# Performance work log

Hardware: AMD Instinct MI355X
Metric: run time of the kernel (lower is better)

## Reference

```python
import jax, jax.numpy as jnp
import numpy as np

N1 = 100000  # source cloud size (x1)
N2 = 100000  # target cloud size (x2)
F = 64       # point feature dim
E = 1600000  # number of radius edges (avg 16 neighbors)
H = 128      # MLP hidden/out dim


def setup_inputs() -> dict:
    key = jax.random.key(0)
    ks = jax.random.split(key, 12)
    s = 0.05
    return {
        "x1_features": jax.random.normal(ks[0], (N1, F), jnp.float32),
        "x1_pos": jax.random.normal(ks[1], (N1, 3), jnp.float32),
        "x2_features": jax.random.normal(ks[2], (N2, F), jnp.float32),
        "x2_pos": jax.random.normal(ks[3], (N2, 3), jnp.float32),
        "W1": jax.random.normal(ks[4], (2 * F + 3, H), jnp.float32) * s,
        "b1": jnp.zeros((H,), jnp.float32),
        "W2": jax.random.normal(ks[5], (H, H), jnp.float32) * s,
        "b2": jnp.zeros((H,), jnp.float32),
        "W3": jax.random.normal(ks[6], (H, H), jnp.float32) * s,
        "b3": jnp.zeros((H,), jnp.float32),
        "edge_src": jax.random.randint(ks[7], (E,), 0, N1, jnp.int32),
        "edge_dst": jax.random.randint(ks[8], (E,), 0, N2, jnp.int32),
    }


def reference(x1_features, x1_pos, x2_features, x2_pos,
              W1, b1, W2, b2, W3, b3, edge_src, edge_dst):
    # message(x_i, x_j, pos_i, pos_j): i = target (x2, edge_dst), j = source (x1, edge_src)
    # msg = cat([x_i, x_j, pos_j - pos_i], dim=1)  -> [E, 2F+3]
    msg = jnp.concatenate(
        [x2_features[edge_dst],
         x1_features[edge_src],
         x1_pos[edge_src] - x2_pos[edge_dst]], axis=1)
    # MLP (Linear+ReLU x3, FastFlow3D make_mlp style)
    h = jax.nn.relu(msg @ W1 + b1)
    h = jax.nn.relu(h @ W2 + b2)
    h = jax.nn.relu(h @ W3 + b3)
    # scatter-max aggregation onto x2 nodes; PyG fills empty segments with 0
    out = jax.ops.segment_max(h, edge_dst, num_segments=N2)
    out = jnp.where(jnp.isneginf(out), 0.0, out)
    return out, x2_pos
```

## Files before the change

kernel.cpp:

```cpp
#include <hip/hip_runtime.h>
#include <hip/hip_bf16.h>

#define DEV __device__ __forceinline__

typedef short bf16x8 __attribute__((ext_vector_type(8)));
typedef float f32x16 __attribute__((ext_vector_type(16)));

static constexpr int FDIM  = 64;
static constexpr int HH    = 128;
static constexpr int K1RAW = 2 * FDIM + 3;
static constexpr int K1    = 144;
static constexpr int KS1   = K1 / 16;
static constexpr int KS2   = HH / 16;
static constexpr int TM    = 128;

static constexpr int CSTR  = TM * 16 + 16;
static constexpr int HCH   = 16;
static constexpr int HBUF  = HCH * CSTR;
static constexpr int L_TOT = 2 * HBUF + TM * 4;

static constexpr int WT1_ELEMS = HH * K1;
static constexpr int WT2_ELEMS = HH * HH;
static constexpr int WT_TOTAL  = WT1_ELEMS + 2 * WT2_ELEMS;

DEV unsigned pack2(float a, float b) {
    union { __hip_bfloat162 h; unsigned u; } cv;
    cv.h.x = __float2bfloat16(a);
    cv.h.y = __float2bfloat16(b);
    return cv.u;
}
DEV unsigned short f2bf(float f) {
    union { __hip_bfloat16 h; unsigned short u; } cv;
    cv.h = __float2bfloat16(f);
    return cv.u;
}

__global__ void k_cvt(const float* __restrict__ src, unsigned short* __restrict__ dst, int n8) {
    int i = blockIdx.x * 256 + threadIdx.x;
    if (i < n8) {
        float4 a = *(const float4*)(src + (size_t)i * 8);
        float4 b = *(const float4*)(src + (size_t)i * 8 + 4);
        uint4 o;
        o.x = pack2(a.x, a.y); o.y = pack2(a.z, a.w);
        o.z = pack2(b.x, b.y); o.w = pack2(b.z, b.w);
        *(uint4*)(dst + (size_t)i * 8) = o;
    }
}

__global__ void k_wprep(const float* __restrict__ W1, const float* __restrict__ W2,
                        const float* __restrict__ W3, unsigned short* __restrict__ wt) {
    int i = blockIdx.x * 256 + threadIdx.x;
    if (i < WT1_ELEMS) {
        int n = i / K1, k = i % K1;
        float v = (k < K1RAW) ? W1[k * HH + n] : 0.f;
        wt[i] = f2bf(v);
    } else if (i < WT1_ELEMS + WT2_ELEMS) {
        int j = i - WT1_ELEMS; int n = j / HH, k = j % HH;
        wt[i] = f2bf(W2[k * HH + n]);
    } else if (i < WT_TOTAL) {
        int j = i - WT1_ELEMS - WT2_ELEMS; int n = j / HH, k = j % HH;
        wt[i] = f2bf(W3[k * HH + n]);
    }
}

__global__ void k_hist(const int* __restrict__ edst, int* __restrict__ cnt, int E) {
    int e = blockIdx.x * 256 + threadIdx.x;
    if (e < E) atomicAdd(&cnt[edst[e]], 1);
}

__global__ void k_scan_part(const int* __restrict__ cnt, int* __restrict__ partial, int n2) {
    __shared__ int sm[256];
    int t = threadIdx.x;
    int base = blockIdx.x * 1024 + t * 4;
    int s = 0;
#pragma unroll
    for (int j = 0; j < 4; j++) { int idx = base + j; if (idx < n2) s += cnt[idx]; }
    sm[t] = s; __syncthreads();
    for (int off = 128; off > 0; off >>= 1) {
        if (t < off) sm[t] += sm[t + off];
        __syncthreads();
    }
    if (t == 0) partial[blockIdx.x] = sm[0];
}

__global__ void k_scan_top(int* __restrict__ partial, int nb) {
    __shared__ int sm[256];
    int t = threadIdx.x;
    int v = (t < nb) ? partial[t] : 0;
    sm[t] = v; __syncthreads();
    for (int off = 1; off < 256; off <<= 1) {
        int add = (t >= off) ? sm[t - off] : 0;
        __syncthreads();
        sm[t] += add;
        __syncthreads();
    }
    if (t < nb) partial[t] = sm[t] - v;
}

__global__ void k_scan_down(const int* __restrict__ cnt, const int* __restrict__ partial,
                            int* __restrict__ cursor, int n2) {
    __shared__ int sm[256];
    int t = threadIdx.x;
    int base = blockIdx.x * 1024 + t * 4;
    int c[4]; int s = 0;
#pragma unroll
    for (int j = 0; j < 4; j++) { int idx = base + j; c[j] = (idx < n2) ? cnt[idx] : 0; s += c[j]; }
    sm[t] = s; __syncthreads();
    for (int off = 1; off < 256; off <<= 1) {
        int add = (t >= off) ? sm[t - off] : 0;
        __syncthreads();
        sm[t] += add;
        __syncthreads();
    }
    int run = partial[blockIdx.x] + (sm[t] - s);
#pragma unroll
    for (int j = 0; j < 4; j++) {
        int idx = base + j;
        if (idx < n2) cursor[idx] = run;
        run += c[j];
    }
}

__global__ void k_fill(const int* __restrict__ edst, const int* __restrict__ esrc,
                       int* __restrict__ cursor,
                       int* __restrict__ csr_s, int* __restrict__ csr_d, int E) {
    int e = blockIdx.x * 256 + threadIdx.x;
    if (e < E) {
        int d = edst[e];
        int p = atomicAdd(&cursor[d], 1);
        csr_s[p] = esrc[e];
        csr_d[p] = d;
    }
}

DEV f32x16 zerov() {
    f32x16 v;
#pragma unroll
    for (int i = 0; i < 16; i++) v[i] = 0.f;
    return v;
}

template <int KSTEPS>
DEV void load_A(const unsigned short* __restrict__ wtl, int rt, int l31, int hh, bf16x8* A) {
#pragma unroll
    for (int ks = 0; ks < KSTEPS; ks++)
        A[ks] = *(const bf16x8*)(wtl + (rt * 32 + l31) * (KSTEPS * 16) + ks * 16 + 8 * hh);
}

template <int KSTEPS>
DEV f32x16 tile_mfma(const bf16x8* A, const char* __restrict__ srcrow) {
    f32x16 acc = zerov();
#pragma unroll
    for (int ks = 0; ks < KSTEPS; ks++) {
        bf16x8 B = *(const bf16x8*)(srcrow + 2 * ks * CSTR);
        acc = __builtin_amdgcn_mfma_f32_32x32x16_bf16(A[ks], B, acc, 0, 0, 0);
    }
    return acc;
}

DEV void tile_store(const f32x16& acc, const float* __restrict__ bias, char* __restrict__ dstrow,
                    int rt, int hh) {
#pragma unroll
    for (int g = 0; g < 4; g++) {
        float4 bv = *(const float4*)(bias + rt * 32 + 8 * g + 4 * hh);
        float v0 = fmaxf(acc[4 * g + 0] + bv.x, 0.f);
        float v1 = fmaxf(acc[4 * g + 1] + bv.y, 0.f);
        float v2 = fmaxf(acc[4 * g + 2] + bv.z, 0.f);
        float v3 = fmaxf(acc[4 * g + 3] + bv.w, 0.f);
        uint2 w; w.x = pack2(v0, v1); w.y = pack2(v2, v3);
        *(uint2*)(dstrow + g * CSTR) = w;
    }
}

template <bool SORTED, bool BF16SRC>
__global__ __launch_bounds__(512, 4) void k_main(
    const float* __restrict__ x1f, const float* __restrict__ x1p,
    const float* __restrict__ x2f, const float* __restrict__ x2p,
    const char* __restrict__ xb1, const char* __restrict__ xb2,
    const float* __restrict__ b1, const float* __restrict__ b2, const float* __restrict__ b3,
    const unsigned short* __restrict__ wt,
    const int* __restrict__ csr_s, const int* __restrict__ csr_d,
    const int* __restrict__ edge_src, const int* __restrict__ edge_dst,
    float* __restrict__ out, int E) {
    __shared__ __align__(16) char sm[L_TOT];
    char* hA = sm;
    char* hB = sm + HBUF;
    int*  dl = (int*)(sm + 2 * HBUF);

    const int tid  = threadIdx.x;
    const int lane = tid & 63;
    const int wv   = tid >> 6;
    const int l31  = lane & 31;
    const int hh   = lane >> 5;
    const int eb   = blockIdx.x * TM;

    if (tid < TM) {
        const int slot = eb + tid;
        dl[tid] = (slot < E) ? (SORTED ? csr_d[slot] : edge_dst[slot]) : -1;
    }

    const int rt  = wv & 3;
    const int ct0 = (wv >> 2) * 2;
    bf16x8 A[KS1];

    load_A<KS1>(wt, rt, l31, hh, A);
#pragma unroll
    for (int j = 0; j < 2; j++) {
        const int r = (ct0 + j) * 32 + l31;
        const int slot = eb + r;
        const bool ok = slot < E;
        int d = 0, s = 0;
        if (ok) {
            d = SORTED ? csr_d[slot] : edge_dst[slot];
            s = SORTED ? csr_s[slot] : edge_src[slot];
        }
        bf16x8 Bv[KS1];
        if (BF16SRC) {
            const char* bx2 = xb2 + (size_t)d * (2 * FDIM);
            const char* bx1 = xb1 + (size_t)s * (2 * FDIM);
#pragma unroll
            for (int ks = 0; ks < 4; ks++)
                Bv[ks] = *(const bf16x8*)(bx2 + (2 * ks + hh) * 16);
#pragma unroll
            for (int ks = 4; ks < 8; ks++)
                Bv[ks] = *(const bf16x8*)(bx1 + (2 * ks + hh) * 16 - 128);
        } else {
            const float* fx2 = x2f + (size_t)d * FDIM;
            const float* fx1 = x1f + (size_t)s * FDIM;
#pragma unroll
            for (int ks = 0; ks < 8; ks++) {
                const float* b = (ks < 4) ? (fx2 + (2 * ks + hh) * 8)
                                          : (fx1 + (2 * ks + hh) * 8 - 64);
                float4 a0 = *(const float4*)(b);
                float4 a1 = *(const float4*)(b + 4);
                union { unsigned u[4]; bf16x8 v; } B;
                B.u[0] = pack2(a0.x, a0.y); B.u[1] = pack2(a0.z, a0.w);
                B.u[2] = pack2(a1.x, a1.y); B.u[3] = pack2(a1.z, a1.w);
                Bv[ks] = B.v;
            }
        }
        {
            float dx = 0.f, dy = 0.f, dz = 0.f;
            if (ok) {
                dx = x1p[s * 3 + 0] - x2p[d * 3 + 0];
                dy = x1p[s * 3 + 1] - x2p[d * 3 + 1];
                dz = x1p[s * 3 + 2] - x2p[d * 3 + 2];
            }
            union { unsigned u[4]; bf16x8 v; } P;
            P.u[0] = hh ? 0u : pack2(dx, dy);
            P.u[1] = hh ? 0u : pack2(dz, 0.f);
            P.u[2] = 0u; P.u[3] = 0u;
            Bv[8] = P.v;
        }
        f32x16 acc = zerov();
#pragma unroll
        for (int ks = 0; ks < KS1; ks++)
            acc = __builtin_amdgcn_mfma_f32_32x32x16_bf16(A[ks], Bv[ks], acc, 0, 0, 0);
        tile_store(acc, b1, hA + r * 16 + 8 * hh + (4 * rt) * CSTR, rt, hh);
    }
    __syncthreads();

    load_A<KS2>(wt + WT1_ELEMS, rt, l31, hh, A);
#pragma unroll
    for (int j = 0; j < 2; j++) {
        const int r = (ct0 + j) * 32 + l31;
        f32x16 acc = tile_mfma<KS2>(A, hA + r * 16 + hh * CSTR);
        tile_store(acc, b2, hB + r * 16 + 8 * hh + (4 * rt) * CSTR, rt, hh);
    }
    __syncthreads();

    load_A<KS2>(wt + WT1_ELEMS + WT2_ELEMS, rt, l31, hh, A);
#pragma unroll
    for (int j = 0; j < 2; j++) {
        const int r = (ct0 + j) * 32 + l31;
        f32x16 acc = tile_mfma<KS2>(A, hB + r * 16 + hh * CSTR);
        tile_store(acc, b3, hA + r * 16 + 8 * hh + (4 * rt) * CSTR, rt, hh);
    }
    __syncthreads();

    {
        const int p     = tid & 63;
        const int strip = tid >> 6;
        const int r0 = strip * 16;
        const char* fbase = hA + (p >> 2) * CSTR + (p & 3) * 4;
        int curd = dl[r0];
        int rs = r0;
        float m0 = 0.f, m1 = 0.f;
#pragma unroll
        for (int r = r0; r < r0 + 16; r++) {
            int d = dl[r];
            if (d != curd) {
                if (curd >= 0) {
                    bool extL = (rs == r0) && (r0 == 0 || dl[r0 - 1] == curd);
                    if (extL) {
                        if (m0 > 0.f) atomicMax((int*)out + (size_t)curd * HH + 2 * p,     __float_as_int(m0));
                        if (m1 > 0.f) atomicMax((int*)out + (size_t)curd * HH + 2 * p + 1, __float_as_int(m1));
                    } else {
                        out[(size_t)curd * HH + 2 * p]     = m0;
                        out[(size_t)curd * HH + 2 * p + 1] = m1;
                    }
                }
                curd = d; rs = r; m0 = 0.f; m1 = 0.f;
            }
            unsigned w = *(const unsigned*)(fbase + r * 16);
            m0 = fmaxf(m0, __uint_as_float(w << 16));
            m1 = fmaxf(m1, __uint_as_float(w & 0xffff0000u));
        }
        if (curd >= 0) {
            bool extL = (rs == r0) && (r0 == 0 || dl[r0 - 1] == curd);
            bool extR = (r0 + 16 == TM) || (dl[r0 + 16] == curd);
            if (extL || extR) {
                if (m0 > 0.f) atomicMax((int*)out + (size_t)curd * HH + 2 * p,     __float_as_int(m0));
                if (m1 > 0.f) atomicMax((int*)out + (size_t)curd * HH + 2 * p + 1, __float_as_int(m1));
            } else {
                out[(size_t)curd * HH + 2 * p]     = m0;
                out[(size_t)curd * HH + 2 * p + 1] = m1;
            }
        }
    }
}

extern "C" void kernel_launch(void* const* d_in, const int* in_sizes, int n_in,
                              void* d_out, int out_size, void* d_ws, size_t ws_size,
                              hipStream_t stream) {
    const float* x1f = (const float*)d_in[0];
    const float* x1p = (const float*)d_in[1];
    const float* x2f = (const float*)d_in[2];
    const float* x2p = (const float*)d_in[3];
    const float* W1  = (const float*)d_in[4];
    const float* b1  = (const float*)d_in[5];
    const float* W2  = (const float*)d_in[6];
    const float* b2  = (const float*)d_in[7];
    const float* W3  = (const float*)d_in[8];
    const float* b3  = (const float*)d_in[9];
    const int* esrc  = (const int*)d_in[10];
    const int* edst  = (const int*)d_in[11];
    const int E  = in_sizes[10];
    const int N1 = in_sizes[1] / 3;
    const int N2 = in_sizes[3] / 3;
    float* out = (float*)d_out;

    size_t off = 0;
    auto take = [&](size_t bytes) { size_t o = off; off = (off + bytes + 255) & ~(size_t)255; return o; };
    size_t o_cnt = take(4 * (size_t)N2);
    size_t o_cur = take(4 * (size_t)N2);
    size_t o_par = take(4 * 256);
    size_t o_cs  = take(4 * (size_t)E);
    size_t o_cd  = take(4 * (size_t)E);
    size_t o_wt  = take(2 * (size_t)WT_TOTAL);
    size_t need_csr = off;
    size_t o_x1  = take(2 * (size_t)N1 * FDIM);
    size_t o_x2  = take(2 * (size_t)N2 * FDIM);
    size_t need_bf = off;

    const int NB = (N2 + 1023) / 1024;
    bool use_csr = (need_csr <= ws_size) && (NB <= 256);
    bool use_bf  = (need_bf <= ws_size);

    char* ws = (char*)d_ws;
    unsigned short* wt = use_csr ? (unsigned short*)(ws + o_wt) : (unsigned short*)ws;
    int* cnt    = (int*)(ws + o_cnt);
    int* cursor = (int*)(ws + o_cur);
    int* part   = (int*)(ws + o_par);
    int* csr_s  = (int*)(ws + o_cs);
    int* csr_d  = (int*)(ws + o_cd);
    char* xb1   = ws + o_x1;
    char* xb2   = ws + o_x2;

    (void)hipMemsetAsync(out, 0, (size_t)N2 * HH * 4, stream);
    (void)hipMemcpyAsync(out + (size_t)N2 * HH, x2p, (size_t)N2 * 3 * 4,
                         hipMemcpyDeviceToDevice, stream);

    k_wprep<<<(WT_TOTAL + 255) / 256, 256, 0, stream>>>(W1, W2, W3, wt);

    if (use_bf) {
        int n8_1 = N1 * FDIM / 8, n8_2 = N2 * FDIM / 8;
        k_cvt<<<(n8_1 + 255) / 256, 256, 0, stream>>>(x1f, (unsigned short*)xb1, n8_1);
        k_cvt<<<(n8_2 + 255) / 256, 256, 0, stream>>>(x2f, (unsigned short*)xb2, n8_2);
    }

    const int grid = (E + TM - 1) / TM;
    if (use_csr) {
        (void)hipMemsetAsync(cnt, 0, 4 * (size_t)N2, stream);
        k_hist<<<(E + 255) / 256, 256, 0, stream>>>(edst, cnt, E);
        k_scan_part<<<NB, 256, 0, stream>>>(cnt, part, N2);
        k_scan_top<<<1, 256, 0, stream>>>(part, NB);
        k_scan_down<<<NB, 256, 0, stream>>>(cnt, part, cursor, N2);
        k_fill<<<(E + 255) / 256, 256, 0, stream>>>(edst, esrc, cursor, csr_s, csr_d, E);
        if (use_bf)
            k_main<true, true><<<grid, 512, 0, stream>>>(
                x1f, x1p, x2f, x2p, xb1, xb2, b1, b2, b3, wt, csr_s, csr_d, esrc, edst, out, E);
        else
            k_main<true, false><<<grid, 512, 0, stream>>>(
                x1f, x1p, x2f, x2p, xb1, xb2, b1, b2, b3, wt, csr_s, csr_d, esrc, edst, out, E);
    } else {
        if (use_bf)
            k_main<false, true><<<grid, 512, 0, stream>>>(
                x1f, x1p, x2f, x2p, xb1, xb2, b1, b2, b3, wt, edst, edst, esrc, edst, out, E);
        else
            k_main<false, false><<<grid, 512, 0, stream>>>(
                x1f, x1p, x2f, x2p, xb1, xb2, b1, b2, b3, wt, edst, edst, esrc, edst, out, E);
    }
}
```

Before: 664.5 us.

## Make main kernel persistent with register-prefetched gathers of the next tile

The main MLP kernel becomes persistent, with a grid capped at 512 blocks looping over edge tiles. Each thread gathers the feature rows for the next tile into registers while the current tile's three MFMA layers run. It then stages the message matrix in shared memory coalesced, with 4 threads per row, instead of gathering straight into MFMA operand registers. The aim is to hide the gather latency behind compute. The cost is extra shared memory (a separate message buffer), more registers, an extra barrier per tile, and fewer resident blocks, which could lower occupancy.

```diff
diff --git a/kernel.cpp b/kernel.cpp
--- a/kernel.cpp
+++ b/kernel.cpp
@@ -15,13 +15,17 @@
 static constexpr int TM    = 128;
 
 static constexpr int CSTR  = TM * 16 + 16;
+static constexpr int MCH   = 18;
+static constexpr int MBUF  = MCH * CSTR;
 static constexpr int HCH   = 16;
 static constexpr int HBUF  = HCH * CSTR;
-static constexpr int L_TOT = 2 * HBUF + TM * 4;
+static constexpr int L_TOT = MBUF + HBUF + TM * 4;
 
 static constexpr int WT1_ELEMS = HH * K1;
 static constexpr int WT2_ELEMS = HH * HH;
 static constexpr int WT_TOTAL  = WT1_ELEMS + 2 * WT2_ELEMS;
+
+static constexpr int NBLK  = 512;
 
 DEV unsigned pack2(float a, float b) {
     union { __hip_bfloat162 h; unsigned u; } cv;
@@ -182,141 +186,172 @@
     const int* __restrict__ csr_s, const int* __restrict__ csr_d,
     const int* __restrict__ edge_src, const int* __restrict__ edge_dst,
     float* __restrict__ out, int E) {
-    __shared__ __align__(16) char sm[L_TOT];
-    char* hA = sm;
-    char* hB = sm + HBUF;
-    int*  dl = (int*)(sm + 2 * HBUF);
+    __shared__ __align__(16) char smem[L_TOT];
+    char* msg = smem;
+    char* hbf = smem + MBUF;
+    int*  dl  = (int*)(smem + MBUF + HBUF);
 
     const int tid  = threadIdx.x;
     const int lane = tid & 63;
     const int wv   = tid >> 6;
     const int l31  = lane & 31;
     const int hh   = lane >> 5;
-    const int eb   = blockIdx.x * TM;
-
-    if (tid < TM) {
-        const int slot = eb + tid;
-        dl[tid] = (slot < E) ? (SORTED ? csr_d[slot] : edge_dst[slot]) : -1;
-    }
-
-    const int rt  = wv & 3;
-    const int ct0 = (wv >> 2) * 2;
-    bf16x8 A[KS1];
-
-    load_A<KS1>(wt, rt, l31, hh, A);
-#pragma unroll
-    for (int j = 0; j < 2; j++) {
-        const int r = (ct0 + j) * 32 + l31;
-        const int slot = eb + r;
-        const bool ok = slot < E;
-        int d = 0, s = 0;
-        if (ok) {
-            d = SORTED ? csr_d[slot] : edge_dst[slot];
-            s = SORTED ? csr_s[slot] : edge_src[slot];
-        }
-        bf16x8 Bv[KS1];
-        if (BF16SRC) {
-            const char* bx2 = xb2 + (size_t)d * (2 * FDIM);
-            const char* bx1 = xb1 + (size_t)s * (2 * FDIM);
-#pragma unroll
-            for (int ks = 0; ks < 4; ks++)
-                Bv[ks] = *(const bf16x8*)(bx2 + (2 * ks + hh) * 16);
-#pragma unroll
-            for (int ks = 4; ks < 8; ks++)
-                Bv[ks] = *(const bf16x8*)(bx1 + (2 * ks + hh) * 16 - 128);
-        } else {
-            const float* fx2 = x2f + (size_t)d * FDIM;
-            const float* fx1 = x1f + (size_t)s * FDIM;
-#pragma unroll
-            for (int ks = 0; ks < 8; ks++) {
-                const float* b = (ks < 4) ? (fx2 + (2 * ks + hh) * 8)
-                                          : (fx1 + (2 * ks + hh) * 8 - 64);
-                float4 a0 = *(const float4*)(b);
-                float4 a1 = *(const float4*)(b + 4);
-                union { unsigned u[4]; bf16x8 v; } B;
-                B.u[0] = pack2(a0.x, a0.y); B.u[1] = pack2(a0.z, a0.w);
-                B.u[2] = pack2(a1.x, a1.y); B.u[3] = pack2(a1.z, a1.w);
-                Bv[ks] = B.v;
-            }
-        }
+    const int r    = tid >> 2;
+    const int sub  = tid & 3;
+    const int rt   = wv & 3;
+    const int ct0  = (wv >> 2) * 2;
+    const int ntiles = (E + TM - 1) / TM;
+    const int nb     = (int)gridDim.x;
+
+    auto load_idx = [&](int tile, int& d, int& s) {
+        const int slot = tile * TM + r;
+        const bool ok = (tile < ntiles) && (slot < E);
+        d = ok ? (SORTED ? csr_d[slot] : edge_dst[slot]) : -1;
+        s = ok ? (SORTED ? csr_s[slot] : edge_src[slot]) : 0;
+    };
+    auto load_feats = [&](int d, int s, uint4* v, float* pp) {
+#pragma unroll
+        for (int i = 0; i < 4; i++) { v[i].x = v[i].y = v[i].z = v[i].w = 0u; }
+        pp[0] = pp[1] = pp[2] = pp[3] = pp[4] = pp[5] = 0.f;
+        if (d >= 0) {
+            if (BF16SRC) {
+                const char* base = (sub < 2) ? (xb2 + (size_t)d * (2 * FDIM))
+                                             : (xb1 + (size_t)s * (2 * FDIM));
+#pragma unroll
+                for (int i = 0; i < 4; i++)
+                    v[i] = *(const uint4*)(base + ((sub & 1) * 4 + i) * 16);
+            } else {
+                const float* base = (sub < 2) ? (x2f + (size_t)d * FDIM)
+                                              : (x1f + (size_t)s * FDIM);
+#pragma unroll
+                for (int i = 0; i < 4; i++) {
+                    const int cc = (sub & 1) * 4 + i;
+                    float4 a = *(const float4*)(base + cc * 8);
+                    float4 b = *(const float4*)(base + cc * 8 + 4);
+                    v[i].x = pack2(a.x, a.y); v[i].y = pack2(a.z, a.w);
+                    v[i].z = pack2(b.x, b.y); v[i].w = pack2(b.z, b.w);
+                }
+            }
+            if (sub == 3) {
+                pp[0] = x1p[s * 3 + 0]; pp[1] = x1p[s * 3 + 1]; pp[2] = x1p[s * 3 + 2];
+                pp[3] = x2p[d * 3 + 0]; pp[4] = x2p[d * 3 + 1]; pp[5] = x2p[d * 3 + 2];
+            }
+        }
+    };
+
+    int tile = (int)blockIdx.x;
+    int d0, s0, d1, s1;
+    uint4 v0[4]; float p0[6];
+    load_idx(tile, d0, s0);
+    load_feats(d0, s0, v0, p0);
+    load_idx(tile + nb, d1, s1);
+
+    for (int t = tile; t < ntiles; t += nb) {
+        __syncthreads();
         {
-            float dx = 0.f, dy = 0.f, dz = 0.f;
-            if (ok) {
-                dx = x1p[s * 3 + 0] - x2p[d * 3 + 0];
-                dy = x1p[s * 3 + 1] - x2p[d * 3 + 1];
-                dz = x1p[s * 3 + 2] - x2p[d * 3 + 2];
-            }
-            union { unsigned u[4]; bf16x8 v; } P;
-            P.u[0] = hh ? 0u : pack2(dx, dy);
-            P.u[1] = hh ? 0u : pack2(dz, 0.f);
-            P.u[2] = 0u; P.u[3] = 0u;
-            Bv[8] = P.v;
-        }
-        f32x16 acc = zerov();
-#pragma unroll
-        for (int ks = 0; ks < KS1; ks++)
-            acc = __builtin_amdgcn_mfma_f32_32x32x16_bf16(A[ks], Bv[ks], acc, 0, 0, 0);
-        tile_store(acc, b1, hA + r * 16 + 8 * hh + (4 * rt) * CSTR, rt, hh);
-    }
-    __syncthreads();
-
-    load_A<KS2>(wt + WT1_ELEMS, rt, l31, hh, A);
-#pragma unroll
-    for (int j = 0; j < 2; j++) {
-        const int r = (ct0 + j) * 32 + l31;
-        f32x16 acc = tile_mfma<KS2>(A, hA + r * 16 + hh * CSTR);
-        tile_store(acc, b2, hB + r * 16 + 8 * hh + (4 * rt) * CSTR, rt, hh);
-    }
-    __syncthreads();
-
-    load_A<KS2>(wt + WT1_ELEMS + WT2_ELEMS, rt, l31, hh, A);
-#pragma unroll
-    for (int j = 0; j < 2; j++) {
-        const int r = (ct0 + j) * 32 + l31;
-        f32x16 acc = tile_mfma<KS2>(A, hB + r * 16 + hh * CSTR);
-        tile_store(acc, b3, hA + r * 16 + 8 * hh + (4 * rt) * CSTR, rt, hh);
-    }
-    __syncthreads();
-
-    {
-        const int p     = tid & 63;
-        const int strip = tid >> 6;
-        const int r0 = strip * 16;
-        const char* fbase = hA + (p >> 2) * CSTR + (p & 3) * 4;
-        int curd = dl[r0];
-        int rs = r0;
-        float m0 = 0.f, m1 = 0.f;
-#pragma unroll
-        for (int r = r0; r < r0 + 16; r++) {
-            int d = dl[r];
-            if (d != curd) {
-                if (curd >= 0) {
-                    bool extL = (rs == r0) && (r0 == 0 || dl[r0 - 1] == curd);
-                    if (extL) {
-                        if (m0 > 0.f) atomicMax((int*)out + (size_t)curd * HH + 2 * p,     __float_as_int(m0));
-                        if (m1 > 0.f) atomicMax((int*)out + (size_t)curd * HH + 2 * p + 1, __float_as_int(m1));
-                    } else {
-                        out[(size_t)curd * HH + 2 * p]     = m0;
-                        out[(size_t)curd * HH + 2 * p + 1] = m1;
+            char* colbase = msg + r * 16 + (sub * 4) * CSTR;
+#pragma unroll
+            for (int i = 0; i < 4; i++)
+                *(uint4*)(colbase + i * CSTR) = v0[i];
+            if (sub == 3) {
+                uint4 v; v.x = pack2(p0[0] - p0[3], p0[1] - p0[4]);
+                v.y = pack2(p0[2] - p0[5], 0.f); v.z = 0u; v.w = 0u;
+                *(uint4*)(msg + r * 16 + 16 * CSTR) = v;
+                uint4 z; z.x = z.y = z.z = z.w = 0u;
+                *(uint4*)(msg + r * 16 + 17 * CSTR) = z;
+            }
+            if (sub == 0) dl[r] = d0;
+        }
+        __syncthreads();
+
+        uint4 v1[4]; float p1[6];
+        load_feats(d1, s1, v1, p1);
+        int d2, s2;
+        load_idx(t + 2 * nb, d2, s2);
+
+        {
+            bf16x8 A[KS1];
+            load_A<KS1>(wt, rt, l31, hh, A);
+#pragma unroll
+            for (int j = 0; j < 2; j++) {
+                const int rr = (ct0 + j) * 32 + l31;
+                f32x16 acc = tile_mfma<KS1>(A, msg + rr * 16 + hh * CSTR);
+                tile_store(acc, b1, hbf + rr * 16 + 8 * hh + (4 * rt) * CSTR, rt, hh);
+            }
+        }
+        __syncthreads();
+
+        {
+            bf16x8 A[KS2];
+            load_A<KS2>(wt + WT1_ELEMS, rt, l31, hh, A);
+#pragma unroll
+            for (int j = 0; j < 2; j++) {
+                const int rr = (ct0 + j) * 32 + l31;
+                f32x16 acc = tile_mfma<KS2>(A, hbf + rr * 16 + hh * CSTR);
+                tile_store(acc, b2, msg + rr * 16 + 8 * hh + (4 * rt) * CSTR, rt, hh);
+            }
+        }
+        __syncthreads();
+
+        {
+            bf16x8 A[KS2];
+            load_A<KS2>(wt + WT1_ELEMS + WT2_ELEMS, rt, l31, hh, A);
+#pragma unroll
+            for (int j = 0; j < 2; j++) {
+                const int rr = (ct0 + j) * 32 + l31;
+                f32x16 acc = tile_mfma<KS2>(A, msg + rr * 16 + hh * CSTR);
+                tile_store(acc, b3, hbf + rr * 16 + 8 * hh + (4 * rt) * CSTR, rt, hh);
+            }
+        }
+        __syncthreads();
+
+        {
+            const int p     = tid & 63;
+            const int strip = tid >> 6;
+            const int r0 = strip * 16;
+            const char* fbase = hbf + (p >> 2) * CSTR + (p & 3) * 4;
+            int curd = dl[r0];
+            int rs = r0;
+            float m0 = 0.f, m1 = 0.f;
+#pragma unroll
+            for (int rr = r0; rr < r0 + 16; rr++) {
+                int d = dl[rr];
+                if (d != curd) {
+                    if (curd >= 0) {
+                        bool extL = (rs == r0) && (r0 == 0 || dl[r0 - 1] == curd);
+                        if (extL) {
+                            if (m0 > 0.f) atomicMax((int*)out + (size_t)curd * HH + 2 * p,     __float_as_int(m0));
+                            if (m1 > 0.f) atomicMax((int*)out + (size_t)curd * HH + 2 * p + 1, __float_as_int(m1));
+                        } else {
+                            out[(size_t)curd * HH + 2 * p]     = m0;
+                            out[(size_t)curd * HH + 2 * p + 1] = m1;
+                        }
                     }
+                    curd = d; rs = rr; m0 = 0.f; m1 = 0.f;
                 }
-                curd = d; rs = r; m0 = 0.f; m1 = 0.f;
-            }
-            unsigned w = *(const unsigned*)(fbase + r * 16);
-            m0 = fmaxf(m0, __uint_as_float(w << 16));
-            m1 = fmaxf(m1, __uint_as_float(w & 0xffff0000u));
-        }
-        if (curd >= 0) {
-            bool extL = (rs == r0) && (r0 == 0 || dl[r0 - 1] == curd);
-            bool extR = (r0 + 16 == TM) || (dl[r0 + 16] == curd);
-            if (extL || extR) {
-                if (m0 > 0.f) atomicMax((int*)out + (size_t)curd * HH + 2 * p,     __float_as_int(m0));
-                if (m1 > 0.f) atomicMax((int*)out + (size_t)curd * HH + 2 * p + 1, __float_as_int(m1));
-            } else {
-                out[(size_t)curd * HH + 2 * p]     = m0;
-                out[(size_t)curd * HH + 2 * p + 1] = m1;
-            }
-        }
+                unsigned w = *(const unsigned*)(fbase + rr * 16);
+                m0 = fmaxf(m0, __uint_as_float(w << 16));
+                m1 = fmaxf(m1, __uint_as_float(w & 0xffff0000u));
+            }
+            if (curd >= 0) {
+                bool extL = (rs == r0) && (r0 == 0 || dl[r0 - 1] == curd);
+                bool extR = (r0 + 16 == TM) || (dl[r0 + 16] == curd);
+                if (extL || extR) {
+                    if (m0 > 0.f) atomicMax((int*)out + (size_t)curd * HH + 2 * p,     __float_as_int(m0));
+                    if (m1 > 0.f) atomicMax((int*)out + (size_t)curd * HH + 2 * p + 1, __float_as_int(m1));
+                } else {
+                    out[(size_t)curd * HH + 2 * p]     = m0;
+                    out[(size_t)curd * HH + 2 * p + 1] = m1;
+                }
+            }
+        }
+
+        d0 = d1; s0 = s1;
+#pragma unroll
+        for (int i = 0; i < 4; i++) v0[i] = v1[i];
+#pragma unroll
+        for (int i = 0; i < 6; i++) p0[i] = p1[i];
+        d1 = d2; s1 = s2;
     }
 }
 
@@ -379,7 +414,8 @@
         k_cvt<<<(n8_2 + 255) / 256, 256, 0, stream>>>(x2f, (unsigned short*)xb2, n8_2);
     }
 
-    const int grid = (E + TM - 1) / TM;
+    const int ntiles = (E + TM - 1) / TM;
+    const int grid = (ntiles < NBLK) ? ntiles : NBLK;
     if (use_csr) {
         (void)hipMemsetAsync(cnt, 0, 4 * (size_t)N2, stream);
         k_hist<<<(E + 255) / 256, 256, 0, stream>>>(edst, cnt, E);
```

New measurement: 1.130 ms. +70.0%, slower.

## Keep MLP activations in registers and fold biases into padded weight columns

Applied to the files above, without the earlier changes.

Each wave now handles 32 edges through all three layers. Inter-layer activations stay in registers and are redistributed with cross-half-wave shuffles instead of round-tripping through LDS with block barriers. Biases are folded into an extra K column of the weight matrices, using a constant-1 input lane in the padded region. The edge tile doubles to 256 per block, with a padded LDS row layout used only for the final scatter-max. The trade-offs are heavier register pressure, weight A-fragments reloaded from global/L2 for every tile, and bias precision reduced to bf16.

```diff
diff --git a/kernel.cpp b/kernel.cpp
--- a/kernel.cpp
+++ b/kernel.cpp
@@ -8,20 +8,16 @@
 
 static constexpr int FDIM  = 64;
 static constexpr int HH    = 128;
-static constexpr int K1RAW = 2 * FDIM + 3;
-static constexpr int K1    = 144;
-static constexpr int KS1   = K1 / 16;
-static constexpr int KS2   = HH / 16;
-static constexpr int TM    = 128;
-
-static constexpr int CSTR  = TM * 16 + 16;
-static constexpr int HCH   = 16;
-static constexpr int HBUF  = HCH * CSTR;
-static constexpr int L_TOT = 2 * HBUF + TM * 4;
-
-static constexpr int WT1_ELEMS = HH * K1;
-static constexpr int WT2_ELEMS = HH * HH;
-static constexpr int WT_TOTAL  = WT1_ELEMS + 2 * WT2_ELEMS;
+static constexpr int KPAD  = 144;
+static constexpr int KS    = KPAD / 16;
+static constexpr int TM    = 256;
+
+static constexpr int CSTR  = TM * 16 + 256 + 16;
+static constexpr int HBUF  = 16 * CSTR;
+static constexpr int L_TOT = HBUF + TM * 4;
+
+static constexpr int WTL      = KPAD * HH;
+static constexpr int WT_TOTAL = 3 * WTL;
 
 DEV unsigned pack2(float a, float b) {
     union { __hip_bfloat162 h; unsigned u; } cv;
@@ -34,6 +30,7 @@
     cv.h = __float2bfloat16(f);
     return cv.u;
 }
+DEV int rowoff(int r) { return r * 16 + (r >> 3) * 8; }
 
 __global__ void k_cvt(const float* __restrict__ src, unsigned short* __restrict__ dst, int n8) {
     int i = blockIdx.x * 256 + threadIdx.x;
@@ -47,20 +44,25 @@
     }
 }
 
-__global__ void k_wprep(const float* __restrict__ W1, const float* __restrict__ W2,
-                        const float* __restrict__ W3, unsigned short* __restrict__ wt) {
+__global__ void k_wprep(const float* __restrict__ W1, const float* __restrict__ b1,
+                        const float* __restrict__ W2, const float* __restrict__ b2,
+                        const float* __restrict__ W3, const float* __restrict__ b3,
+                        unsigned short* __restrict__ wt) {
     int i = blockIdx.x * 256 + threadIdx.x;
-    if (i < WT1_ELEMS) {
-        int n = i / K1, k = i % K1;
-        float v = (k < K1RAW) ? W1[k * HH + n] : 0.f;
-        wt[i] = f2bf(v);
-    } else if (i < WT1_ELEMS + WT2_ELEMS) {
-        int j = i - WT1_ELEMS; int n = j / HH, k = j % HH;
-        wt[i] = f2bf(W2[k * HH + n]);
-    } else if (i < WT_TOTAL) {
-        int j = i - WT1_ELEMS - WT2_ELEMS; int n = j / HH, k = j % HH;
-        wt[i] = f2bf(W3[k * HH + n]);
-    }
+    if (i >= WT_TOTAL) return;
+    int layer = i / WTL, j = i % WTL;
+    int n = j / KPAD, k = j % KPAD;
+    float v = 0.f;
+    if (layer == 0) {
+        if (k < 131) v = W1[k * HH + n];
+        else if (k == 131) v = b1[n];
+    } else {
+        const float* W = (layer == 1) ? W2 : W3;
+        const float* b = (layer == 1) ? b2 : b3;
+        if (k < 128) v = W[k * HH + n];
+        else if (k == 128) v = b[n];
+    }
+    wt[i] = f2bf(v);
 }
 
 __global__ void k_hist(const int* __restrict__ edst, int* __restrict__ cnt, int E) {
@@ -139,36 +141,42 @@
     for (int i = 0; i < 16; i++) v[i] = 0.f;
     return v;
 }
-
-template <int KSTEPS>
-DEV void load_A(const unsigned short* __restrict__ wtl, int rt, int l31, int hh, bf16x8* A) {
-#pragma unroll
-    for (int ks = 0; ks < KSTEPS; ks++)
-        A[ks] = *(const bf16x8*)(wtl + (rt * 32 + l31) * (KSTEPS * 16) + ks * 16 + 8 * hh);
-}
-
-template <int KSTEPS>
-DEV f32x16 tile_mfma(const bf16x8* A, const char* __restrict__ srcrow) {
-    f32x16 acc = zerov();
-#pragma unroll
-    for (int ks = 0; ks < KSTEPS; ks++) {
-        bf16x8 B = *(const bf16x8*)(srcrow + 2 * ks * CSTR);
-        acc = __builtin_amdgcn_mfma_f32_32x32x16_bf16(A[ks], B, acc, 0, 0, 0);
-    }
-    return acc;
-}
-
-DEV void tile_store(const f32x16& acc, const float* __restrict__ bias, char* __restrict__ dstrow,
-                    int rt, int hh) {
-#pragma unroll
-    for (int g = 0; g < 4; g++) {
-        float4 bv = *(const float4*)(bias + rt * 32 + 8 * g + 4 * hh);
-        float v0 = fmaxf(acc[4 * g + 0] + bv.x, 0.f);
-        float v1 = fmaxf(acc[4 * g + 1] + bv.y, 0.f);
-        float v2 = fmaxf(acc[4 * g + 2] + bv.z, 0.f);
-        float v3 = fmaxf(acc[4 * g + 3] + bv.w, 0.f);
-        uint2 w; w.x = pack2(v0, v1); w.y = pack2(v2, v3);
-        *(uint2*)(dstrow + g * CSTR) = w;
+DEV float relu(float x) { return fmaxf(x, 0.f); }
+
+DEV void layer_reg(const unsigned short* __restrict__ wtl, const unsigned pkin[32],
+                   unsigned pkout[32], int l31, int hh, unsigned biasw) {
+    unsigned xv[16];
+#pragma unroll
+    for (int ks = 0; ks < 8; ks++) {
+        unsigned t0 = hh ? pkin[4 * ks + 0] : pkin[4 * ks + 2];
+        unsigned t1 = hh ? pkin[4 * ks + 1] : pkin[4 * ks + 3];
+        xv[2 * ks + 0] = (unsigned)__shfl_xor((int)t0, 32, 64);
+        xv[2 * ks + 1] = (unsigned)__shfl_xor((int)t1, 32, 64);
+    }
+#pragma unroll
+    for (int rt = 0; rt < 4; rt++) {
+        f32x16 acc = zerov();
+#pragma unroll
+        for (int ks = 0; ks < 8; ks++) {
+            union { unsigned u[4]; bf16x8 v; } B;
+            B.u[0] = hh ? xv[2 * ks + 0]   : pkin[4 * ks + 0];
+            B.u[1] = hh ? xv[2 * ks + 1]   : pkin[4 * ks + 1];
+            B.u[2] = hh ? pkin[4 * ks + 2] : xv[2 * ks + 0];
+            B.u[3] = hh ? pkin[4 * ks + 3] : xv[2 * ks + 1];
+            bf16x8 A = *(const bf16x8*)(wtl + (rt * 32 + l31) * KPAD + ks * 16 + 8 * hh);
+            acc = __builtin_amdgcn_mfma_f32_32x32x16_bf16(A, B.v, acc, 0, 0, 0);
+        }
+        {
+            union { unsigned u[4]; bf16x8 v; } B;
+            B.u[0] = biasw; B.u[1] = 0u; B.u[2] = 0u; B.u[3] = 0u;
+            bf16x8 A = *(const bf16x8*)(wtl + (rt * 32 + l31) * KPAD + 8 * 16 + 8 * hh);
+            acc = __builtin_amdgcn_mfma_f32_32x32x16_bf16(A, B.v, acc, 0, 0, 0);
+        }
+#pragma unroll
+        for (int g = 0; g < 4; g++) {
+            pkout[8 * rt + 2 * g + 0] = pack2(relu(acc[4 * g + 0]), relu(acc[4 * g + 1]));
+            pkout[8 * rt + 2 * g + 1] = pack2(relu(acc[4 * g + 2]), relu(acc[4 * g + 3]));
+        }
     }
 }
 
@@ -177,15 +185,13 @@
     const float* __restrict__ x1f, const float* __restrict__ x1p,
     const float* __restrict__ x2f, const float* __restrict__ x2p,
     const char* __restrict__ xb1, const char* __restrict__ xb2,
-    const float* __restrict__ b1, const float* __restrict__ b2, const float* __restrict__ b3,
     const unsigned short* __restrict__ wt,
     const int* __restrict__ csr_s, const int* __restrict__ csr_d,
     const int* __restrict__ edge_src, const int* __restrict__ edge_dst,
     float* __restrict__ out, int E) {
-    __shared__ __align__(16) char sm[L_TOT];
-    char* hA = sm;
-    char* hB = sm + HBUF;
-    int*  dl = (int*)(sm + 2 * HBUF);
+    __shared__ __align__(16) char smem[L_TOT];
+    char* hbf = smem;
+    int*  dl  = (int*)(smem + HBUF);
 
     const int tid  = threadIdx.x;
     const int lane = tid & 63;
@@ -193,103 +199,98 @@
     const int l31  = lane & 31;
     const int hh   = lane >> 5;
     const int eb   = blockIdx.x * TM;
-
-    if (tid < TM) {
-        const int slot = eb + tid;
-        dl[tid] = (slot < E) ? (SORTED ? csr_d[slot] : edge_dst[slot]) : -1;
-    }
-
-    const int rt  = wv & 3;
-    const int ct0 = (wv >> 2) * 2;
-    bf16x8 A[KS1];
-
-    load_A<KS1>(wt, rt, l31, hh, A);
-#pragma unroll
-    for (int j = 0; j < 2; j++) {
-        const int r = (ct0 + j) * 32 + l31;
-        const int slot = eb + r;
-        const bool ok = slot < E;
-        int d = 0, s = 0;
+    const int r    = wv * 32 + l31;
+    const int slot = eb + r;
+    const bool ok  = slot < E;
+
+    int d = 0, s = 0;
+    if (ok) {
+        d = SORTED ? csr_d[slot] : edge_dst[slot];
+        s = SORTED ? csr_s[slot] : edge_src[slot];
+    }
+    if (hh == 0) dl[r] = ok ? d : -1;
+
+    bf16x8 Bv[KS];
+    if (BF16SRC) {
+        const char* bx2 = xb2 + (size_t)d * (2 * FDIM);
+        const char* bx1 = xb1 + (size_t)s * (2 * FDIM);
+#pragma unroll
+        for (int ks = 0; ks < 4; ks++)
+            Bv[ks] = *(const bf16x8*)(bx2 + (2 * ks + hh) * 16);
+#pragma unroll
+        for (int ks = 4; ks < 8; ks++)
+            Bv[ks] = *(const bf16x8*)(bx1 + (2 * (ks - 4) + hh) * 16);
+    } else {
+        const float* fx2 = x2f + (size_t)d * FDIM;
+        const float* fx1 = x1f + (size_t)s * FDIM;
+#pragma unroll
+        for (int ks = 0; ks < 8; ks++) {
+            const float* b = (ks < 4) ? (fx2 + (2 * ks + hh) * 8)
+                                      : (fx1 + (2 * (ks - 4) + hh) * 8);
+            float4 a0 = *(const float4*)(b);
+            float4 a1 = *(const float4*)(b + 4);
+            union { unsigned u[4]; bf16x8 v; } B;
+            B.u[0] = pack2(a0.x, a0.y); B.u[1] = pack2(a0.z, a0.w);
+            B.u[2] = pack2(a1.x, a1.y); B.u[3] = pack2(a1.z, a1.w);
+            Bv[ks] = B.v;
+        }
+    }
+    {
+        float dx = 0.f, dy = 0.f, dz = 0.f;
         if (ok) {
-            d = SORTED ? csr_d[slot] : edge_dst[slot];
-            s = SORTED ? csr_s[slot] : edge_src[slot];
-        }
-        bf16x8 Bv[KS1];
-        if (BF16SRC) {
-            const char* bx2 = xb2 + (size_t)d * (2 * FDIM);
-            const char* bx1 = xb1 + (size_t)s * (2 * FDIM);
-#pragma unroll
-            for (int ks = 0; ks < 4; ks++)
-                Bv[ks] = *(const bf16x8*)(bx2 + (2 * ks + hh) * 16);
-#pragma unroll
-            for (int ks = 4; ks < 8; ks++)
-                Bv[ks] = *(const bf16x8*)(bx1 + (2 * ks + hh) * 16 - 128);
-        } else {
-            const float* fx2 = x2f + (size_t)d * FDIM;
-            const float* fx1 = x1f + (size_t)s * FDIM;
-#pragma unroll
-            for (int ks = 0; ks < 8; ks++) {
-                const float* b = (ks < 4) ? (fx2 + (2 * ks + hh) * 8)
-                                          : (fx1 + (2 * ks + hh) * 8 - 64);
-                float4 a0 = *(const float4*)(b);
-                float4 a1 = *(const float4*)(b + 4);
-                union { unsigned u[4]; bf16x8 v; } B;
-                B.u[0] = pack2(a0.x, a0.y); B.u[1] = pack2(a0.z, a0.w);
-                B.u[2] = pack2(a1.x, a1.y); B.u[3] = pack2(a1.z, a1.w);
-                Bv[ks] = B.v;
-            }
-        }
-        {
-            float dx = 0.f, dy = 0.f, dz = 0.f;
-            if (ok) {
-                dx = x1p[s * 3 + 0] - x2p[d * 3 + 0];
-                dy = x1p[s * 3 + 1] - x2p[d * 3 + 1];
-                dz = x1p[s * 3 + 2] - x2p[d * 3 + 2];
-            }
-            union { unsigned u[4]; bf16x8 v; } P;
-            P.u[0] = hh ? 0u : pack2(dx, dy);
-            P.u[1] = hh ? 0u : pack2(dz, 0.f);
-            P.u[2] = 0u; P.u[3] = 0u;
-            Bv[8] = P.v;
-        }
+            dx = x1p[s * 3 + 0] - x2p[d * 3 + 0];
+            dy = x1p[s * 3 + 1] - x2p[d * 3 + 1];
+            dz = x1p[s * 3 + 2] - x2p[d * 3 + 2];
+        }
+        union { unsigned u[4]; bf16x8 v; } P;
+        P.u[0] = hh ? 0u : pack2(dx, dy);
+        P.u[1] = hh ? 0u : pack2(dz, 1.0f);
+        P.u[2] = 0u; P.u[3] = 0u;
+        Bv[8] = P.v;
+    }
+
+    unsigned pkA[32], pkB[32];
+#pragma unroll
+    for (int rt = 0; rt < 4; rt++) {
         f32x16 acc = zerov();
 #pragma unroll
-        for (int ks = 0; ks < KS1; ks++)
-            acc = __builtin_amdgcn_mfma_f32_32x32x16_bf16(A[ks], Bv[ks], acc, 0, 0, 0);
-        tile_store(acc, b1, hA + r * 16 + 8 * hh + (4 * rt) * CSTR, rt, hh);
-    }
-    __syncthreads();
-
-    load_A<KS2>(wt + WT1_ELEMS, rt, l31, hh, A);
-#pragma unroll
-    for (int j = 0; j < 2; j++) {
-        const int r = (ct0 + j) * 32 + l31;
-        f32x16 acc = tile_mfma<KS2>(A, hA + r * 16 + hh * CSTR);
-        tile_store(acc, b2, hB + r * 16 + 8 * hh + (4 * rt) * CSTR, rt, hh);
-    }
-    __syncthreads();
-
-    load_A<KS2>(wt + WT1_ELEMS + WT2_ELEMS, rt, l31, hh, A);
-#pragma unroll
-    for (int j = 0; j < 2; j++) {
-        const int r = (ct0 + j) * 32 + l31;
-        f32x16 acc = tile_mfma<KS2>(A, hB + r * 16 + hh * CSTR);
-        tile_store(acc, b3, hA + r * 16 + 8 * hh + (4 * rt) * CSTR, rt, hh);
+        for (int ks = 0; ks < KS; ks++) {
+            bf16x8 A = *(const bf16x8*)(wt + (rt * 32 + l31) * KPAD + ks * 16 + 8 * hh);
+            acc = __builtin_amdgcn_mfma_f32_32x32x16_bf16(A, Bv[ks], acc, 0, 0, 0);
+        }
+#pragma unroll
+        for (int g = 0; g < 4; g++) {
+            pkA[8 * rt + 2 * g + 0] = pack2(relu(acc[4 * g + 0]), relu(acc[4 * g + 1]));
+            pkA[8 * rt + 2 * g + 1] = pack2(relu(acc[4 * g + 2]), relu(acc[4 * g + 3]));
+        }
+    }
+
+    const unsigned biasw = hh ? 0u : 0x00003F80u;
+    layer_reg(wt + WTL,     pkA, pkB, l31, hh, biasw);
+    layer_reg(wt + 2 * WTL, pkB, pkA, l31, hh, biasw);
+
+    {
+        char* dst = hbf + rowoff(r) + 8 * hh;
+#pragma unroll
+        for (int u = 0; u < 16; u++) {
+            uint2 w; w.x = pkA[2 * u + 0]; w.y = pkA[2 * u + 1];
+            *(uint2*)(dst + u * CSTR) = w;
+        }
     }
     __syncthreads();
 
     {
         const int p     = tid & 63;
         const int strip = tid >> 6;
-        const int r0 = strip * 16;
-        const char* fbase = hA + (p >> 2) * CSTR + (p & 3) * 4;
+        const int r0 = strip * 32;
+        const char* fbase = hbf + (p >> 2) * CSTR + (p & 3) * 4;
         int curd = dl[r0];
         int rs = r0;
         float m0 = 0.f, m1 = 0.f;
-#pragma unroll
-        for (int r = r0; r < r0 + 16; r++) {
-            int d = dl[r];
-            if (d != curd) {
+#pragma unroll 4
+        for (int rr = r0; rr < r0 + 32; rr++) {
+            int dd = dl[rr];
+            if (dd != curd) {
                 if (curd >= 0) {
                     bool extL = (rs == r0) && (r0 == 0 || dl[r0 - 1] == curd);
                     if (extL) {
@@ -300,15 +301,15 @@
                         out[(size_t)curd * HH + 2 * p + 1] = m1;
                     }
                 }
-                curd = d; rs = r; m0 = 0.f; m1 = 0.f;
+                curd = dd; rs = rr; m0 = 0.f; m1 = 0.f;
             }
-            unsigned w = *(const unsigned*)(fbase + r * 16);
+            unsigned w = *(const unsigned*)(fbase + rowoff(rr));
             m0 = fmaxf(m0, __uint_as_float(w << 16));
             m1 = fmaxf(m1, __uint_as_float(w & 0xffff0000u));
         }
         if (curd >= 0) {
             bool extL = (rs == r0) && (r0 == 0 || dl[r0 - 1] == curd);
-            bool extR = (r0 + 16 == TM) || (dl[r0 + 16] == curd);
+            bool extR = (r0 + 32 == TM) || (dl[r0 + 32] == curd);
             if (extL || extR) {
                 if (m0 > 0.f) atomicMax((int*)out + (size_t)curd * HH + 2 * p,     __float_as_int(m0));
                 if (m1 > 0.f) atomicMax((int*)out + (size_t)curd * HH + 2 * p + 1, __float_as_int(m1));
@@ -371,7 +372,7 @@
     (void)hipMemcpyAsync(out + (size_t)N2 * HH, x2p, (size_t)N2 * 3 * 4,
                          hipMemcpyDeviceToDevice, stream);
 
-    k_wprep<<<(WT_TOTAL + 255) / 256, 256, 0, stream>>>(W1, W2, W3, wt);
+    k_wprep<<<(WT_TOTAL + 255) / 256, 256, 0, stream>>>(W1, b1, W2, b2, W3, b3, wt);
 
     if (use_bf) {
         int n8_1 = N1 * FDIM / 8, n8_2 = N2 * FDIM / 8;
@@ -389,16 +390,16 @@
         k_fill<<<(E + 255) / 256, 256, 0, stream>>>(edst, esrc, cursor, csr_s, csr_d, E);
         if (use_bf)
             k_main<true, true><<<grid, 512, 0, stream>>>(
-                x1f, x1p, x2f, x2p, xb1, xb2, b1, b2, b3, wt, csr_s, csr_d, esrc, edst, out, E);
+                x1f, x1p, x2f, x2p, xb1, xb2, wt, csr_s, csr_d, esrc, edst, out, E);
         else
             k_main<true, false><<<grid, 512, 0, stream>>>(
-                x1f, x1p, x2f, x2p, xb1, xb2, b1, b2, b3, wt, csr_s, csr_d, esrc, edst, out, E);
+                x1f, x1p, x2f, x2p, xb1, xb2, wt, csr_s, csr_d, esrc, edst, out, E);
     } else {
         if (use_bf)
             k_main<false, true><<<grid, 512, 0, stream>>>(
-                x1f, x1p, x2f, x2p, xb1, xb2, b1, b2, b3, wt, edst, edst, esrc, edst, out, E);
+                x1f, x1p, x2f, x2p, xb1, xb2, wt, edst, edst, esrc, edst, out, E);
         else
             k_main<false, false><<<grid, 512, 0, stream>>>(
-                x1f, x1p, x2f, x2p, xb1, xb2, b1, b2, b3, wt, edst, edst, esrc, edst, out, E);
-    }
-}
+                x1f, x1p, x2f, x2p, xb1, xb2, wt, edst, edst, esrc, edst, out, E);
+    }
+}
```

Result: faster. 616.0 us (-7.3%).
